# Performance work log

Hardware: AMD Instinct MI355X
Metric: run time of the kernel (lower is better)

The kernel has to match this reference:

```python
import jax, jax.numpy as jnp
import numpy as np


def conv2d(x, w, b, stride=1, pad=0):
    out = jax.lax.conv_general_dilated(
        x, w, (stride, stride), ((pad, pad), (pad, pad)),
        dimension_numbers=('NCHW', 'OIHW', 'NCHW'))
    return out + b[None, :, None, None]


def maxpool2(x):
    return jax.lax.reduce_window(x, -jnp.inf, jax.lax.max,
                                 (1, 1, 2, 2), (1, 1, 2, 2), 'VALID')


def pixel_match_(x, y):
    # x, y: (1, C, H, W). 9-way shifted squared-diff cost volume.
    _, C, H, W = x.shape
    yc = y[0, :, 1:H - 1, 1:W - 1]
    inner = []
    for dh in range(3):
        for dw in range(3):
            tmp = x[0, :, dh:dh + H - 2, dw:dw + W - 2] - yc
            inner.append(jnp.sum(tmp * tmp, axis=0))
    inner = jnp.stack(inner)  # (9, H-2, W-2)
    diff = jnp.zeros((9, H, W), x.dtype).at[:, 1:H - 1, 1:W - 1].set(inner)
    diff = 1.0 / jnp.sqrt(diff + 0.01)
    diff = diff / jnp.sum(diff, axis=0, keepdims=True)
    return diff[None]  # (1, 9, H, W)


def positional(H, W, dtype):
    h = jnp.arange(H, dtype=dtype)
    w = jnp.arange(W, dtype=dtype)
    h = 2.0 * h / h[-1] - 1.0
    w = 2.0 * w / w[-1] - 1.0
    ph = jnp.broadcast_to(h[:, None], (H, W))
    pw = jnp.broadcast_to(w[None, :], (H, W))
    return jnp.stack([ph, pw])[None]  # (1, 2, H, W)


def pixel_match(x, y):
    return jnp.concatenate(
        [pixel_match_(x, y), pixel_match_(y, x),
         positional(x.shape[2], x.shape[3], x.dtype)], axis=1)


def adaptive_max_pool3(x):
    # torch adaptive_max_pool2d semantics: bin i spans [floor(i*H/3), ceil((i+1)*H/3))
    _, C, H, W = x.shape
    rows = []
    for i in range(3):
        hs, he = (i * H) // 3, -((-(i + 1) * H) // 3)
        cols = []
        for j in range(3):
            ws, we = (j * W) // 3, -((-(j + 1) * W) // 3)
            cols.append(jnp.max(x[:, :, hs:he, ws:we], axis=(2, 3)))
        rows.append(jnp.stack(cols, axis=-1))
    return jnp.stack(rows, axis=-2)  # (1, C, 3, 3)


def setup_inputs() -> dict:
    key = jax.random.key(0)
    ks = jax.random.split(key, 16)
    f = jnp.float32
    H = W = 1024
    s = 0.05
    return {
        'x1': jax.random.normal(ks[0], (3, H, W), f),
        'x2': jax.random.normal(ks[1], (3, H, W), f),
        'enc_w': jax.random.normal(ks[2], (24, 3, 3, 3), f) * s,
        'enc_b': jax.random.normal(ks[3], (24,), f) * s,
        'embed_w': jax.random.normal(ks[4], (32, 24, 1, 1), f) * s,
        'embed_b': jax.random.normal(ks[5], (32,), f) * s,
        'dense_w': jax.random.normal(ks[6], (8, 32, 5, 5), f) * s,
        'dense_b': jax.random.normal(ks[7], (8,), f) * s,
        'f1_w': jax.random.normal(ks[8], (64, 48, 1, 1), f) * s,
        'f1_b': jax.random.normal(ks[9], (64,), f) * s,
        'f2_w': jax.random.normal(ks[10], (128, 64, 3, 3), f) * s,
        'f2_b': jax.random.normal(ks[11], (128,), f) * s,
        'f3_w': jax.random.normal(ks[12], (6, 128), f) * s,
        'f3_b': jax.random.normal(ks[13], (6,), f) * s,
    }


def reference(x1, x2, enc_w, enc_b, embed_w, embed_b, dense_w, dense_b,
              f1_w, f1_b, f2_w, f2_b, f3_w, f3_b):
    def coding(x):
        x = x[None]  # (1,3,H,W)
        x = jax.lax.stop_gradient(conv2d(x, enc_w, enc_b, pad=1))  # frozen encoder
        x = conv2d(x, embed_w, embed_b)
        return maxpool2(x)

    c1 = coding(x1)
    c2 = coding(x2)
    level1 = maxpool2(pixel_match(c1, c2))
    p1 = maxpool2(c1)
    p2 = maxpool2(c2)
    level2 = pixel_match(p1, p2)
    dense = jax.nn.leaky_relu(conv2d(p1 - p2, dense_w, dense_b, pad=2))
    x = jnp.concatenate([level1, level2, dense], axis=1)  # (1,48,H/4,W/4)
    x = conv2d(x, f1_w, f1_b)
    x = adaptive_max_pool3(x)
    x = conv2d(x, f2_w, f2_b).reshape(1, 128)
    tmp = jnp.sum(x * x) + 0.001
    x = x / jnp.sqrt(tmp)
    x = (x @ f3_w.T + f3_b).reshape(2, 3)
    x = jnp.concatenate([x, jnp.zeros((1, 3), x.dtype)], axis=0)
    return jnp.eye(3, dtype=x.dtype) + jnp.clip(x, -0.11, 0.11) + x * 0.01
```

## Files before the change

### kernel.cpp

```cpp
#include <hip/hip_runtime.h>
#include <math.h>


__global__ void fuse_weights_kernel(const float* __restrict__ enc_w,
                                    const float* __restrict__ enc_b,
                                    const float* __restrict__ embed_w,
                                    const float* __restrict__ embed_b,
                                    float* __restrict__ weff_t,
                                    float* __restrict__ beff) {
    int t = threadIdx.x;
    for (int idx = t; idx < 27 * 32; idx += blockDim.x) {
        int r = idx >> 5, o = idx & 31;
        float s = 0.f;
        for (int k = 0; k < 24; ++k) s += embed_w[o * 24 + k] * enc_w[k * 27 + r];
        weff_t[idx] = s;
    }
    if (t < 32) {
        float s = embed_b[t];
        for (int k = 0; k < 24; ++k) s += embed_w[t * 24 + k] * enc_b[k];
        beff[t] = s;
    }
}

__global__ __launch_bounds__(256) void coding_kernel(
    const float* __restrict__ x1, const float* __restrict__ x2,
    const float* __restrict__ weff_t, const float* __restrict__ beff,
    float* __restrict__ c1, float* __restrict__ c2,
    float* __restrict__ p1, float* __restrict__ p2) {
    int tx = threadIdx.x, ty = threadIdx.y;
    int img = blockIdx.z;
    const float* x = img ? x2 : x1;
    float* c = img ? c2 : c1;
    float* p = img ? p2 : p1;
    int Y = blockIdx.y * 16 + ty;
    int cx = blockIdx.x * 16 + tx;
    int X0 = 2 * cx;
    bool interior = (blockIdx.y > 0 && blockIdx.y < 63 &&
                     blockIdx.x > 0 && blockIdx.x < 31);
    float acc0[32], acc1[32];
#pragma unroll
    for (int o = 0; o < 32; ++o) {
        acc0[o] = beff[o];
        acc1[o] = acc0[o];
    }
#pragma unroll 1
    for (int ci = 0; ci < 3; ++ci) {
        float in[3][4];
        const float* xc = x + ci * 1048576;
        if (interior) {
#pragma unroll
            for (int r = 0; r < 3; ++r) {
                const float* row = xc + (Y - 1 + r) * 1024 + X0 - 1;
#pragma unroll
                for (int q = 0; q < 4; ++q) in[r][q] = row[q];
            }
        } else {
#pragma unroll
            for (int r = 0; r < 3; ++r)
#pragma unroll
                for (int q = 0; q < 4; ++q) {
                    int gy = Y - 1 + r, gx = X0 - 1 + q;
                    in[r][q] = (gy >= 0 && gy < 1024 && gx >= 0 && gx < 1024)
                                   ? xc[gy * 1024 + gx]
                                   : 0.f;
                }
        }
#pragma unroll
        for (int ky = 0; ky < 3; ++ky)
#pragma unroll
            for (int kx = 0; kx < 3; ++kx) {
                const float* wrow = weff_t + (ci * 9 + ky * 3 + kx) * 32;
                float xa = in[ky][kx];
                float xb = in[ky][kx + 1];
#pragma unroll
                for (int o = 0; o < 32; ++o) {
                    float wv = wrow[o];
                    acc0[o] = fmaf(wv, xa, acc0[o]);
                    acc1[o] = fmaf(wv, xb, acc1[o]);
                }
            }
    }
#pragma unroll
    for (int o = 0; o < 32; ++o) {
        float m = fmaxf(acc0[o], acc1[o]);
        acc0[o] = fmaxf(m, __shfl_xor(m, 16, 64));
    }
    int cpix = (Y >> 1) * 512 + cx;
    if ((ty & 1) == 0) {
        float4* cd = (float4*)(c + cpix * 32);
#pragma unroll
        for (int q = 0; q < 8; ++q)
            cd[q] = make_float4(acc0[4 * q], acc0[4 * q + 1], acc0[4 * q + 2],
                                acc0[4 * q + 3]);
    }
#pragma unroll
    for (int o = 0; o < 32; ++o) {
        float v = fmaxf(acc0[o], __shfl_xor(acc0[o], 1, 64));
        acc0[o] = fmaxf(v, __shfl_xor(v, 32, 64));
    }
    if (((ty & 3) == 0) && ((tx & 1) == 0)) {
        int ppix = (Y >> 2) * 256 + (cx >> 1);
        float4* pd = (float4*)(p + ppix * 32);
#pragma unroll
        for (int q = 0; q < 8; ++q)
            pd[q] = make_float4(acc0[4 * q], acc0[4 * q + 1], acc0[4 * q + 2],
                                acc0[4 * q + 3]);
    }
}

__global__ __launch_bounds__(256) void pm512_pool_kernel(
    const float* __restrict__ c1, const float* __restrict__ c2,
    float* __restrict__ feat) {
    int tid = threadIdx.x;
    int quad = tid & 3;
    int pl = tid >> 2;
    int px = pl & 7, py = pl >> 3;
    int sw = blockIdx.x * 8 + px;
    int sh = blockIdx.y * 8 + py;
    bool interior = (sh >= 1 && sh <= 510 && sw >= 1 && sw <= 510);
    const float* b1 = c1 + (sh * 512 + sw) * 32 + quad * 8;
    const float* b2 = c2 + (sh * 512 + sw) * 32 + quad * 8;
    float a1[9], a2[9];
#pragma unroll
    for (int k = 0; k < 9; ++k) { a1[k] = 0.f; a2[k] = 0.f; }
    if (interior) {
        float4 y1a = ((const float4*)b1)[0], y1b = ((const float4*)b1)[1];
        float4 y2a = ((const float4*)b2)[0], y2b = ((const float4*)b2)[1];
#pragma unroll
        for (int dh = -1; dh <= 1; ++dh)
#pragma unroll
            for (int dw = -1; dw <= 1; ++dw) {
                int k = (dh + 1) * 3 + (dw + 1);
                const float4* n1 = (const float4*)(b1 + (dh * 512 + dw) * 32);
                const float4* n2 = (const float4*)(b2 + (dh * 512 + dw) * 32);
                float4 na = n1[0], nA = n1[1], nb = n2[0], nB = n2[1];
                float s1 = a1[k], s2 = a2[k], t;
                t = na.x - y2a.x; s1 = fmaf(t, t, s1);
                t = na.y - y2a.y; s1 = fmaf(t, t, s1);
                t = na.z - y2a.z; s1 = fmaf(t, t, s1);
                t = na.w - y2a.w; s1 = fmaf(t, t, s1);
                t = nA.x - y2b.x; s1 = fmaf(t, t, s1);
                t = nA.y - y2b.y; s1 = fmaf(t, t, s1);
                t = nA.z - y2b.z; s1 = fmaf(t, t, s1);
                t = nA.w - y2b.w; s1 = fmaf(t, t, s1);
                t = nb.x - y1a.x; s2 = fmaf(t, t, s2);
                t = nb.y - y1a.y; s2 = fmaf(t, t, s2);
                t = nb.z - y1a.z; s2 = fmaf(t, t, s2);
                t = nb.w - y1a.w; s2 = fmaf(t, t, s2);
                t = nB.x - y1b.x; s2 = fmaf(t, t, s2);
                t = nB.y - y1b.y; s2 = fmaf(t, t, s2);
                t = nB.z - y1b.z; s2 = fmaf(t, t, s2);
                t = nB.w - y1b.w; s2 = fmaf(t, t, s2);
                a1[k] = s1;
                a2[k] = s2;
            }
    }
#pragma unroll
    for (int k = 0; k < 9; ++k) {
        a1[k] += __shfl_xor(a1[k], 1, 64);
        a1[k] += __shfl_xor(a1[k], 2, 64);
        a2[k] += __shfl_xor(a2[k], 1, 64);
        a2[k] += __shfl_xor(a2[k], 2, 64);
    }
    float d[20];
    if (interior) {
        float s1 = 0.f, s2 = 0.f;
#pragma unroll
        for (int k = 0; k < 9; ++k) {
            a1[k] = 1.0f / sqrtf(a1[k] + 0.01f);
            a2[k] = 1.0f / sqrtf(a2[k] + 0.01f);
            s1 += a1[k];
            s2 += a2[k];
        }
        float i1 = 1.0f / s1, i2 = 1.0f / s2;
#pragma unroll
        for (int k = 0; k < 9; ++k) {
            d[k] = a1[k] * i1;
            d[9 + k] = a2[k] * i2;
        }
    } else {
#pragma unroll
        for (int k = 0; k < 18; ++k) d[k] = 1.0f / 9.0f;
    }
#pragma unroll
    for (int k = 0; k < 18; ++k) {
        float v = fmaxf(d[k], __shfl_xor(d[k], 4, 64));
        d[k] = fmaxf(v, __shfl_xor(v, 32, 64));
    }
    d[18] = 2.0f * (sh | 1) / 511.0f - 1.0f;
    d[19] = 2.0f * (sw | 1) / 511.0f - 1.0f;
    if ((tid & 36) == 0) {
        int opix = (sh >> 1) * 256 + (sw >> 1);
#pragma unroll
        for (int j = 0; j < 5; ++j)
            feat[(quad * 5 + j) * 65536 + opix] = d[quad * 5 + j];
    }
}

__global__ __launch_bounds__(256) void pm256_kernel(
    const float* __restrict__ p1, const float* __restrict__ p2,
    float* __restrict__ feat) {
    int tid = threadIdx.x;
    int quad = tid & 3;
    int pl = tid >> 2;
    int px = pl & 7, py = pl >> 3;
    int w = blockIdx.x * 8 + px;
    int h = blockIdx.y * 8 + py;
    bool interior = (h >= 1 && h <= 254 && w >= 1 && w <= 254);
    const float* b1 = p1 + (h * 256 + w) * 32 + quad * 8;
    const float* b2 = p2 + (h * 256 + w) * 32 + quad * 8;
    float a1[9], a2[9];
#pragma unroll
    for (int k = 0; k < 9; ++k) { a1[k] = 0.f; a2[k] = 0.f; }
    if (interior) {
        float4 y1a = ((const float4*)b1)[0], y1b = ((const float4*)b1)[1];
        float4 y2a = ((const float4*)b2)[0], y2b = ((const float4*)b2)[1];
#pragma unroll
        for (int dh = -1; dh <= 1; ++dh)
#pragma unroll
            for (int dw = -1; dw <= 1; ++dw) {
                int k = (dh + 1) * 3 + (dw + 1);
                const float4* n1 = (const float4*)(b1 + (dh * 256 + dw) * 32);
                const float4* n2 = (const float4*)(b2 + (dh * 256 + dw) * 32);
                float4 na = n1[0], nA = n1[1], nb = n2[0], nB = n2[1];
                float s1 = a1[k], s2 = a2[k], t;
                t = na.x - y2a.x; s1 = fmaf(t, t, s1);
                t = na.y - y2a.y; s1 = fmaf(t, t, s1);
                t = na.z - y2a.z; s1 = fmaf(t, t, s1);
                t = na.w - y2a.w; s1 = fmaf(t, t, s1);
                t = nA.x - y2b.x; s1 = fmaf(t, t, s1);
                t = nA.y - y2b.y; s1 = fmaf(t, t, s1);
                t = nA.z - y2b.z; s1 = fmaf(t, t, s1);
                t = nA.w - y2b.w; s1 = fmaf(t, t, s1);
                t = nb.x - y1a.x; s2 = fmaf(t, t, s2);
                t = nb.y - y1a.y; s2 = fmaf(t, t, s2);
                t = nb.z - y1a.z; s2 = fmaf(t, t, s2);
                t = nb.w - y1a.w; s2 = fmaf(t, t, s2);
                t = nB.x - y1b.x; s2 = fmaf(t, t, s2);
                t = nB.y - y1b.y; s2 = fmaf(t, t, s2);
                t = nB.z - y1b.z; s2 = fmaf(t, t, s2);
                t = nB.w - y1b.w; s2 = fmaf(t, t, s2);
                a1[k] = s1;
                a2[k] = s2;
            }
    }
#pragma unroll
    for (int k = 0; k < 9; ++k) {
        a1[k] += __shfl_xor(a1[k], 1, 64);
        a1[k] += __shfl_xor(a1[k], 2, 64);
        a2[k] += __shfl_xor(a2[k], 1, 64);
        a2[k] += __shfl_xor(a2[k], 2, 64);
    }
    float d[20];
    if (interior) {
        float s1 = 0.f, s2 = 0.f;
#pragma unroll
        for (int k = 0; k < 9; ++k) {
            a1[k] = 1.0f / sqrtf(a1[k] + 0.01f);
            a2[k] = 1.0f / sqrtf(a2[k] + 0.01f);
            s1 += a1[k];
            s2 += a2[k];
        }
        float i1 = 1.0f / s1, i2 = 1.0f / s2;
#pragma unroll
        for (int k = 0; k < 9; ++k) {
            d[k] = a1[k] * i1;
            d[9 + k] = a2[k] * i2;
        }
    } else {
#pragma unroll
        for (int k = 0; k < 18; ++k) d[k] = 1.0f / 9.0f;
    }
    d[18] = 2.0f * h / 255.0f - 1.0f;
    d[19] = 2.0f * w / 255.0f - 1.0f;
    int pix = h * 256 + w;
#pragma unroll
    for (int j = 0; j < 5; ++j)
        feat[(20 + quad * 5 + j) * 65536 + pix] = d[quad * 5 + j];
}

__global__ __launch_bounds__(256) void dense_part_kernel(
    const float* __restrict__ p1, const float* __restrict__ p2,
    const float* __restrict__ dw, float* __restrict__ part) {
    __shared__ float sdiff[4 * 1296];
    __shared__ float sw[4 * 8 * 28];
    int tx = threadIdx.x, ty = threadIdx.y;
    int tid = ty * 16 + tx;
    int bz = blockIdx.z;
    int h0 = blockIdx.y * 32, w0 = blockIdx.x * 32;
    for (int idx = tid; idx < 1296; idx += 256) {
        int yy = idx / 36, xx = idx % 36;
        int gy = h0 + yy - 2, gx = w0 + xx - 2;
        float4 dv = make_float4(0.f, 0.f, 0.f, 0.f);
        if (gy >= 0 && gy < 256 && gx >= 0 && gx < 256) {
            const float4* q1 =
                (const float4*)(p1 + (gy * 256 + gx) * 32 + bz * 4);
            const float4* q2 =
                (const float4*)(p2 + (gy * 256 + gx) * 32 + bz * 4);
            float4 v1 = q1[0], v2 = q2[0];
            dv = make_float4(v1.x - v2.x, v1.y - v2.y, v1.z - v2.z, v1.w - v2.w);
        }
        sdiff[0 * 1296 + idx] = dv.x;
        sdiff[1 * 1296 + idx] = dv.y;
        sdiff[2 * 1296 + idx] = dv.z;
        sdiff[3 * 1296 + idx] = dv.w;
    }
    for (int idx = tid; idx < 4 * 8 * 28; idx += 256) {
        int ci = idx / 224, r = idx % 224;
        int o = r / 28, k = r % 28;
        sw[idx] = (k < 25) ? dw[o * 800 + (bz * 4 + ci) * 25 + k] : 0.f;
    }
    __syncthreads();
    float acc[4][8];
#pragma unroll
    for (int pq = 0; pq < 4; ++pq)
#pragma unroll
        for (int o = 0; o < 8; ++o) acc[pq][o] = 0.f;
    for (int ci = 0; ci < 4; ++ci) {
        float patch[6][6];
#pragma unroll
        for (int yy = 0; yy < 6; ++yy) {
            const float* rowp = &sdiff[ci * 1296 + (2 * ty + yy) * 36 + 2 * tx];
#pragma unroll
            for (int cpair = 0; cpair < 3; ++cpair) {
                float2 lp = *(const float2*)&rowp[2 * cpair];
                patch[yy][2 * cpair] = lp.x;
                patch[yy][2 * cpair + 1] = lp.y;
            }
        }
#pragma unroll
        for (int o = 0; o < 8; ++o) {
            float wreg[28];
            const float4* wp = (const float4*)&sw[(ci * 8 + o) * 28];
#pragma unroll
            for (int q = 0; q < 7; ++q) {
                float4 wv = wp[q];
                wreg[4 * q] = wv.x;
                wreg[4 * q + 1] = wv.y;
                wreg[4 * q + 2] = wv.z;
                wreg[4 * q + 3] = wv.w;
            }
#pragma unroll
            for (int ky = 0; ky < 5; ++ky)
#pragma unroll
                for (int kx = 0; kx < 5; ++kx) {
                    float wv = wreg[ky * 5 + kx];
#pragma unroll
                    for (int pq = 0; pq < 4; ++pq)
                        acc[pq][o] = fmaf(
                            wv, patch[ky + (pq >> 1)][kx + (pq & 1)], acc[pq][o]);
                }
        }
    }
#pragma unroll
    for (int pq = 0; pq < 4; ++pq) {
        int h = h0 + 2 * ty + (pq >> 1), w = w0 + 2 * tx + (pq & 1);
        int pix = h * 256 + w;
#pragma unroll
        for (int o = 0; o < 8; ++o)
            part[bz * 524288 + o * 65536 + pix] = acc[pq][o];
    }
}

__global__ __launch_bounds__(256) void dense_reduce_kernel(
    const float* __restrict__ part, const float* __restrict__ db,
    float* __restrict__ feat) {
    int idx = blockIdx.x * 256 + threadIdx.x;
    int o = idx >> 16;
    float s = db[o];
#pragma unroll
    for (int z = 0; z < 8; ++z) s += part[z * 524288 + idx];
    float v = (s >= 0.f) ? s : 0.01f * s;
    feat[40 * 65536 + idx] = v;
}

__global__ __launch_bounds__(256) void f1_kernel(
    const float* __restrict__ feat, const float* __restrict__ f1w,
    const float* __restrict__ f1b, float* __restrict__ out) {
    __shared__ float sw[1536];
    __shared__ float sb[32];
    int og = blockIdx.y;
    int tid = threadIdx.x;
    for (int i = tid; i < 1536; i += 256) sw[i] = f1w[og * 1536 + i];
    if (tid < 32) sb[tid] = f1b[og * 32 + tid];
    __syncthreads();
    int pix = blockIdx.x * 256 + tid;
    float f[48];
#pragma unroll
    for (int c = 0; c < 48; ++c) f[c] = feat[c * 65536 + pix];
#pragma unroll
    for (int o = 0; o < 32; ++o) {
        float a = sb[o];
        const float4* wv = (const float4*)&sw[o * 48];
#pragma unroll
        for (int c4 = 0; c4 < 12; ++c4) {
            float4 ww = wv[c4];
            a = fmaf(ww.x, f[c4 * 4], a);
            a = fmaf(ww.y, f[c4 * 4 + 1], a);
            a = fmaf(ww.z, f[c4 * 4 + 2], a);
            a = fmaf(ww.w, f[c4 * 4 + 3], a);
        }
        out[(og * 32 + o) * 65536 + pix] = a;
    }
}

__global__ __launch_bounds__(256) void pool3_kernel(
    const float* __restrict__ f1out, float* __restrict__ pooled) {
    int b = blockIdx.x;
    int c = b / 9, ij = b % 9, i = ij / 3, j = ij % 3;
    int hs = (i * 256) / 3, he = ((i + 1) * 256 + 2) / 3;
    int ws = (j * 256) / 3, we = ((j + 1) * 256 + 2) / 3;
    const float* src = f1out + c * 65536;
    int nh = he - hs, nw = we - ws, tot = nh * nw;
    float m = -INFINITY;
    for (int t = threadIdx.x; t < tot; t += 256) {
        int r = t / nw, q = t - r * nw;
        m = fmaxf(m, src[(hs + r) * 256 + (ws + q)]);
    }
    for (int off = 32; off > 0; off >>= 1) m = fmaxf(m, __shfl_down(m, off, 64));
    __shared__ float red[4];
    if ((threadIdx.x & 63) == 0) red[threadIdx.x >> 6] = m;
    __syncthreads();
    if (threadIdx.x == 0)
        pooled[b] = fmaxf(fmaxf(red[0], red[1]), fmaxf(red[2], red[3]));
}

__global__ __launch_bounds__(128) void final_kernel(
    const float* __restrict__ pooled, const float* __restrict__ f2w,
    const float* __restrict__ f2b, const float* __restrict__ f3w,
    const float* __restrict__ f3b, float* __restrict__ out) {
    __shared__ float xn[128];
    __shared__ float red[2];
    __shared__ float ov[6];
    int t = threadIdx.x;
    float a = f2b[t];
    for (int c = 0; c < 64; ++c)
#pragma unroll
        for (int k = 0; k < 9; ++k)
            a = fmaf(f2w[t * 576 + c * 9 + k], pooled[c * 9 + k], a);
    float sq = a * a;
    for (int off = 32; off > 0; off >>= 1) sq += __shfl_down(sq, off, 64);
    if ((t & 63) == 0) red[t >> 6] = sq;
    __syncthreads();
    float tmp = red[0] + red[1] + 0.001f;
    float scale = 1.0f / sqrtf(tmp);
    xn[t] = a * scale;
    __syncthreads();
    if (t < 6) {
        float o = f3b[t];
        for (int k = 0; k < 128; ++k) o = fmaf(f3w[t * 128 + k], xn[k], o);
        ov[t] = o;
    }
    __syncthreads();
    if (t < 9) {
        int r = t / 3, cc = t % 3;
        float v = 0.f;
        if (r < 2) {
            float x = ov[r * 3 + cc];
            float cl = fminf(fmaxf(x, -0.11f), 0.11f);
            v = cl + 0.01f * x;
        }
        if (r == cc) v += 1.0f;
        out[t] = v;
    }
}

extern "C" void kernel_launch(void* const* d_in, const int* in_sizes, int n_in,
                              void* d_out, int out_size, void* d_ws,
                              size_t ws_size, hipStream_t stream) {
    const float* x1 = (const float*)d_in[0];
    const float* x2 = (const float*)d_in[1];
    const float* enc_w = (const float*)d_in[2];
    const float* enc_b = (const float*)d_in[3];
    const float* embed_w = (const float*)d_in[4];
    const float* embed_b = (const float*)d_in[5];
    const float* dense_w = (const float*)d_in[6];
    const float* dense_b = (const float*)d_in[7];
    const float* f1_w = (const float*)d_in[8];
    const float* f1_b = (const float*)d_in[9];
    const float* f2_w = (const float*)d_in[10];
    const float* f2_b = (const float*)d_in[11];
    const float* f3_w = (const float*)d_in[12];
    const float* f3_b = (const float*)d_in[13];

    float* ws = (float*)d_ws;
    float* weff_t = ws;
    float* beff = ws + 864;
    float* c1 = ws + 1024;
    float* c2 = c1 + 8388608;
    float* p1 = c2 + 8388608;
    float* p2 = p1 + 2097152;
    float* feat = p2 + 2097152;
    float* pooled = feat + 3145728;
    float* f1o = c1;
    float* part = c2;

    fuse_weights_kernel<<<1, 256, 0, stream>>>(enc_w, enc_b, embed_w, embed_b,
                                               weff_t, beff);
    coding_kernel<<<dim3(32, 64, 2), dim3(16, 16), 0, stream>>>(
        x1, x2, weff_t, beff, c1, c2, p1, p2);
    pm512_pool_kernel<<<dim3(64, 64), 256, 0, stream>>>(c1, c2, feat);
    pm256_kernel<<<dim3(32, 32), 256, 0, stream>>>(p1, p2, feat);
    dense_part_kernel<<<dim3(8, 8, 8), dim3(16, 16), 0, stream>>>(
        p1, p2, dense_w, part);
    dense_reduce_kernel<<<2048, 256, 0, stream>>>(part, dense_b, feat);
    f1_kernel<<<dim3(256, 2), 256, 0, stream>>>(feat, f1_w, f1_b, f1o);
    pool3_kernel<<<576, 256, 0, stream>>>(f1o, pooled);
    final_kernel<<<1, 128, 0, stream>>>(pooled, f2_w, f2_b, f3_w, f3_b,
                                        (float*)d_out);
}
```

Measured before the change: 184.9 us.

## Merge pixel-match and dense conv into one launch; fold dense reduce into f1

Combines the 512-level pixel-match, the 256-level pixel-match and the dense partial-conv kernels into a single kernel that dispatches on block index, so three launches become one and their blocks can run together. The dense reduction with bias and leaky-relu moves into f1_kernel, which now sums the 8 partial buffers itself instead of reading a precomputed feature plane. The partial buffer moves to its own workspace region because it can no longer alias c2, which the fused kernel still reads. The cost is that every block reserves the dense path's shared memory, which may lower occupancy for the pixel-match blocks, and f1 does extra reads (each output-group block re-reads the partials).

```diff
diff --git a/kernel.cpp b/kernel.cpp
--- a/kernel.cpp
+++ b/kernel.cpp
@@ -108,274 +108,272 @@
     }
 }
 
-__global__ __launch_bounds__(256) void pm512_pool_kernel(
+__global__ __launch_bounds__(256) void mid_kernel(
     const float* __restrict__ c1, const float* __restrict__ c2,
-    float* __restrict__ feat) {
+    const float* __restrict__ p1, const float* __restrict__ p2,
+    const float* __restrict__ dw, float* __restrict__ feat,
+    float* __restrict__ part) {
+    __shared__ float smem[4 * 1296 + 4 * 8 * 28];
+    int bid = blockIdx.x;
     int tid = threadIdx.x;
-    int quad = tid & 3;
-    int pl = tid >> 2;
-    int px = pl & 7, py = pl >> 3;
-    int sw = blockIdx.x * 8 + px;
-    int sh = blockIdx.y * 8 + py;
-    bool interior = (sh >= 1 && sh <= 510 && sw >= 1 && sw <= 510);
-    const float* b1 = c1 + (sh * 512 + sw) * 32 + quad * 8;
-    const float* b2 = c2 + (sh * 512 + sw) * 32 + quad * 8;
-    float a1[9], a2[9];
-#pragma unroll
-    for (int k = 0; k < 9; ++k) { a1[k] = 0.f; a2[k] = 0.f; }
-    if (interior) {
-        float4 y1a = ((const float4*)b1)[0], y1b = ((const float4*)b1)[1];
-        float4 y2a = ((const float4*)b2)[0], y2b = ((const float4*)b2)[1];
-#pragma unroll
-        for (int dh = -1; dh <= 1; ++dh)
-#pragma unroll
-            for (int dw = -1; dw <= 1; ++dw) {
-                int k = (dh + 1) * 3 + (dw + 1);
-                const float4* n1 = (const float4*)(b1 + (dh * 512 + dw) * 32);
-                const float4* n2 = (const float4*)(b2 + (dh * 512 + dw) * 32);
-                float4 na = n1[0], nA = n1[1], nb = n2[0], nB = n2[1];
-                float s1 = a1[k], s2 = a2[k], t;
-                t = na.x - y2a.x; s1 = fmaf(t, t, s1);
-                t = na.y - y2a.y; s1 = fmaf(t, t, s1);
-                t = na.z - y2a.z; s1 = fmaf(t, t, s1);
-                t = na.w - y2a.w; s1 = fmaf(t, t, s1);
-                t = nA.x - y2b.x; s1 = fmaf(t, t, s1);
-                t = nA.y - y2b.y; s1 = fmaf(t, t, s1);
-                t = nA.z - y2b.z; s1 = fmaf(t, t, s1);
-                t = nA.w - y2b.w; s1 = fmaf(t, t, s1);
-                t = nb.x - y1a.x; s2 = fmaf(t, t, s2);
-                t = nb.y - y1a.y; s2 = fmaf(t, t, s2);
-                t = nb.z - y1a.z; s2 = fmaf(t, t, s2);
-                t = nb.w - y1a.w; s2 = fmaf(t, t, s2);
-                t = nB.x - y1b.x; s2 = fmaf(t, t, s2);
-                t = nB.y - y1b.y; s2 = fmaf(t, t, s2);
-                t = nB.z - y1b.z; s2 = fmaf(t, t, s2);
-                t = nB.w - y1b.w; s2 = fmaf(t, t, s2);
-                a1[k] = s1;
-                a2[k] = s2;
-            }
-    }
-#pragma unroll
-    for (int k = 0; k < 9; ++k) {
-        a1[k] += __shfl_xor(a1[k], 1, 64);
-        a1[k] += __shfl_xor(a1[k], 2, 64);
-        a2[k] += __shfl_xor(a2[k], 1, 64);
-        a2[k] += __shfl_xor(a2[k], 2, 64);
-    }
-    float d[20];
-    if (interior) {
-        float s1 = 0.f, s2 = 0.f;
+    if (bid < 4096) {
+        int bx = bid & 63, by = bid >> 6;
+        int quad = tid & 3;
+        int pl = tid >> 2;
+        int px = pl & 7, py = pl >> 3;
+        int sw = bx * 8 + px;
+        int sh = by * 8 + py;
+        bool interior = (sh >= 1 && sh <= 510 && sw >= 1 && sw <= 510);
+        const float* b1 = c1 + (sh * 512 + sw) * 32 + quad * 8;
+        const float* b2 = c2 + (sh * 512 + sw) * 32 + quad * 8;
+        float a1[9], a2[9];
+#pragma unroll
+        for (int k = 0; k < 9; ++k) { a1[k] = 0.f; a2[k] = 0.f; }
+        if (interior) {
+            float4 y1a = ((const float4*)b1)[0], y1b = ((const float4*)b1)[1];
+            float4 y2a = ((const float4*)b2)[0], y2b = ((const float4*)b2)[1];
+#pragma unroll
+            for (int dh = -1; dh <= 1; ++dh)
+#pragma unroll
+                for (int dwp = -1; dwp <= 1; ++dwp) {
+                    int k = (dh + 1) * 3 + (dwp + 1);
+                    const float4* n1 =
+                        (const float4*)(b1 + (dh * 512 + dwp) * 32);
+                    const float4* n2 =
+                        (const float4*)(b2 + (dh * 512 + dwp) * 32);
+                    float4 na = n1[0], nA = n1[1], nb = n2[0], nB = n2[1];
+                    float s1 = a1[k], s2 = a2[k], t;
+                    t = na.x - y2a.x; s1 = fmaf(t, t, s1);
+                    t = na.y - y2a.y; s1 = fmaf(t, t, s1);
+                    t = na.z - y2a.z; s1 = fmaf(t, t, s1);
+                    t = na.w - y2a.w; s1 = fmaf(t, t, s1);
+                    t = nA.x - y2b.x; s1 = fmaf(t, t, s1);
+                    t = nA.y - y2b.y; s1 = fmaf(t, t, s1);
+                    t = nA.z - y2b.z; s1 = fmaf(t, t, s1);
+                    t = nA.w - y2b.w; s1 = fmaf(t, t, s1);
+                    t = nb.x - y1a.x; s2 = fmaf(t, t, s2);
+                    t = nb.y - y1a.y; s2 = fmaf(t, t, s2);
+                    t = nb.z - y1a.z; s2 = fmaf(t, t, s2);
+                    t = nb.w - y1a.w; s2 = fmaf(t, t, s2);
+                    t = nB.x - y1b.x; s2 = fmaf(t, t, s2);
+                    t = nB.y - y1b.y; s2 = fmaf(t, t, s2);
+                    t = nB.z - y1b.z; s2 = fmaf(t, t, s2);
+                    t = nB.w - y1b.w; s2 = fmaf(t, t, s2);
+                    a1[k] = s1;
+                    a2[k] = s2;
+                }
+        }
 #pragma unroll
         for (int k = 0; k < 9; ++k) {
-            a1[k] = 1.0f / sqrtf(a1[k] + 0.01f);
-            a2[k] = 1.0f / sqrtf(a2[k] + 0.01f);
-            s1 += a1[k];
-            s2 += a2[k];
-        }
-        float i1 = 1.0f / s1, i2 = 1.0f / s2;
+            a1[k] += __shfl_xor(a1[k], 1, 64);
+            a1[k] += __shfl_xor(a1[k], 2, 64);
+            a2[k] += __shfl_xor(a2[k], 1, 64);
+            a2[k] += __shfl_xor(a2[k], 2, 64);
+        }
+        float d[20];
+        if (interior) {
+            float s1 = 0.f, s2 = 0.f;
+#pragma unroll
+            for (int k = 0; k < 9; ++k) {
+                a1[k] = 1.0f / sqrtf(a1[k] + 0.01f);
+                a2[k] = 1.0f / sqrtf(a2[k] + 0.01f);
+                s1 += a1[k];
+                s2 += a2[k];
+            }
+            float i1 = 1.0f / s1, i2 = 1.0f / s2;
+#pragma unroll
+            for (int k = 0; k < 9; ++k) {
+                d[k] = a1[k] * i1;
+                d[9 + k] = a2[k] * i2;
+            }
+        } else {
+#pragma unroll
+            for (int k = 0; k < 18; ++k) d[k] = 1.0f / 9.0f;
+        }
+#pragma unroll
+        for (int k = 0; k < 18; ++k) {
+            float v = fmaxf(d[k], __shfl_xor(d[k], 4, 64));
+            d[k] = fmaxf(v, __shfl_xor(v, 32, 64));
+        }
+        d[18] = 2.0f * (sh | 1) / 511.0f - 1.0f;
+        d[19] = 2.0f * (sw | 1) / 511.0f - 1.0f;
+        if ((tid & 36) == 0) {
+            int opix = (sh >> 1) * 256 + (sw >> 1);
+#pragma unroll
+            for (int j = 0; j < 5; ++j)
+                feat[(quad * 5 + j) * 65536 + opix] = d[quad * 5 + j];
+        }
+    } else if (bid < 5120) {
+        int i = bid - 4096;
+        int bx = i & 31, by = i >> 5;
+        int quad = tid & 3;
+        int pl = tid >> 2;
+        int px = pl & 7, py = pl >> 3;
+        int w = bx * 8 + px;
+        int h = by * 8 + py;
+        bool interior = (h >= 1 && h <= 254 && w >= 1 && w <= 254);
+        const float* b1 = p1 + (h * 256 + w) * 32 + quad * 8;
+        const float* b2 = p2 + (h * 256 + w) * 32 + quad * 8;
+        float a1[9], a2[9];
+#pragma unroll
+        for (int k = 0; k < 9; ++k) { a1[k] = 0.f; a2[k] = 0.f; }
+        if (interior) {
+            float4 y1a = ((const float4*)b1)[0], y1b = ((const float4*)b1)[1];
+            float4 y2a = ((const float4*)b2)[0], y2b = ((const float4*)b2)[1];
+#pragma unroll
+            for (int dh = -1; dh <= 1; ++dh)
+#pragma unroll
+                for (int dwp = -1; dwp <= 1; ++dwp) {
+                    int k = (dh + 1) * 3 + (dwp + 1);
+                    const float4* n1 =
+                        (const float4*)(b1 + (dh * 256 + dwp) * 32);
+                    const float4* n2 =
+                        (const float4*)(b2 + (dh * 256 + dwp) * 32);
+                    float4 na = n1[0], nA = n1[1], nb = n2[0], nB = n2[1];
+                    float s1 = a1[k], s2 = a2[k], t;
+                    t = na.x - y2a.x; s1 = fmaf(t, t, s1);
+                    t = na.y - y2a.y; s1 = fmaf(t, t, s1);
+                    t = na.z - y2a.z; s1 = fmaf(t, t, s1);
+                    t = na.w - y2a.w; s1 = fmaf(t, t, s1);
+                    t = nA.x - y2b.x; s1 = fmaf(t, t, s1);
+                    t = nA.y - y2b.y; s1 = fmaf(t, t, s1);
+                    t = nA.z - y2b.z; s1 = fmaf(t, t, s1);
+                    t = nA.w - y2b.w; s1 = fmaf(t, t, s1);
+                    t = nb.x - y1a.x; s2 = fmaf(t, t, s2);
+                    t = nb.y - y1a.y; s2 = fmaf(t, t, s2);
+                    t = nb.z - y1a.z; s2 = fmaf(t, t, s2);
+                    t = nb.w - y1a.w; s2 = fmaf(t, t, s2);
+                    t = nB.x - y1b.x; s2 = fmaf(t, t, s2);
+                    t = nB.y - y1b.y; s2 = fmaf(t, t, s2);
+                    t = nB.z - y1b.z; s2 = fmaf(t, t, s2);
+                    t = nB.w - y1b.w; s2 = fmaf(t, t, s2);
+                    a1[k] = s1;
+                    a2[k] = s2;
+                }
+        }
 #pragma unroll
         for (int k = 0; k < 9; ++k) {
-            d[k] = a1[k] * i1;
-            d[9 + k] = a2[k] * i2;
-        }
+            a1[k] += __shfl_xor(a1[k], 1, 64);
+            a1[k] += __shfl_xor(a1[k], 2, 64);
+            a2[k] += __shfl_xor(a2[k], 1, 64);
+            a2[k] += __shfl_xor(a2[k], 2, 64);
+        }
+        float d[20];
+        if (interior) {
+            float s1 = 0.f, s2 = 0.f;
+#pragma unroll
+            for (int k = 0; k < 9; ++k) {
+                a1[k] = 1.0f / sqrtf(a1[k] + 0.01f);
+                a2[k] = 1.0f / sqrtf(a2[k] + 0.01f);
+                s1 += a1[k];
+                s2 += a2[k];
+            }
+            float i1 = 1.0f / s1, i2 = 1.0f / s2;
+#pragma unroll
+            for (int k = 0; k < 9; ++k) {
+                d[k] = a1[k] * i1;
+                d[9 + k] = a2[k] * i2;
+            }
+        } else {
+#pragma unroll
+            for (int k = 0; k < 18; ++k) d[k] = 1.0f / 9.0f;
+        }
+        d[18] = 2.0f * h / 255.0f - 1.0f;
+        d[19] = 2.0f * w / 255.0f - 1.0f;
+        int pix = h * 256 + w;
+#pragma unroll
+        for (int j = 0; j < 5; ++j)
+            feat[(20 + quad * 5 + j) * 65536 + pix] = d[quad * 5 + j];
     } else {
-#pragma unroll
-        for (int k = 0; k < 18; ++k) d[k] = 1.0f / 9.0f;
-    }
-#pragma unroll
-    for (int k = 0; k < 18; ++k) {
-        float v = fmaxf(d[k], __shfl_xor(d[k], 4, 64));
-        d[k] = fmaxf(v, __shfl_xor(v, 32, 64));
-    }
-    d[18] = 2.0f * (sh | 1) / 511.0f - 1.0f;
-    d[19] = 2.0f * (sw | 1) / 511.0f - 1.0f;
-    if ((tid & 36) == 0) {
-        int opix = (sh >> 1) * 256 + (sw >> 1);
-#pragma unroll
-        for (int j = 0; j < 5; ++j)
-            feat[(quad * 5 + j) * 65536 + opix] = d[quad * 5 + j];
-    }
-}
-
-__global__ __launch_bounds__(256) void pm256_kernel(
-    const float* __restrict__ p1, const float* __restrict__ p2,
-    float* __restrict__ feat) {
-    int tid = threadIdx.x;
-    int quad = tid & 3;
-    int pl = tid >> 2;
-    int px = pl & 7, py = pl >> 3;
-    int w = blockIdx.x * 8 + px;
-    int h = blockIdx.y * 8 + py;
-    bool interior = (h >= 1 && h <= 254 && w >= 1 && w <= 254);
-    const float* b1 = p1 + (h * 256 + w) * 32 + quad * 8;
-    const float* b2 = p2 + (h * 256 + w) * 32 + quad * 8;
-    float a1[9], a2[9];
-#pragma unroll
-    for (int k = 0; k < 9; ++k) { a1[k] = 0.f; a2[k] = 0.f; }
-    if (interior) {
-        float4 y1a = ((const float4*)b1)[0], y1b = ((const float4*)b1)[1];
-        float4 y2a = ((const float4*)b2)[0], y2b = ((const float4*)b2)[1];
-#pragma unroll
-        for (int dh = -1; dh <= 1; ++dh)
-#pragma unroll
-            for (int dw = -1; dw <= 1; ++dw) {
-                int k = (dh + 1) * 3 + (dw + 1);
-                const float4* n1 = (const float4*)(b1 + (dh * 256 + dw) * 32);
-                const float4* n2 = (const float4*)(b2 + (dh * 256 + dw) * 32);
-                float4 na = n1[0], nA = n1[1], nb = n2[0], nB = n2[1];
-                float s1 = a1[k], s2 = a2[k], t;
-                t = na.x - y2a.x; s1 = fmaf(t, t, s1);
-                t = na.y - y2a.y; s1 = fmaf(t, t, s1);
-                t = na.z - y2a.z; s1 = fmaf(t, t, s1);
-                t = na.w - y2a.w; s1 = fmaf(t, t, s1);
-                t = nA.x - y2b.x; s1 = fmaf(t, t, s1);
-                t = nA.y - y2b.y; s1 = fmaf(t, t, s1);
-                t = nA.z - y2b.z; s1 = fmaf(t, t, s1);
-                t = nA.w - y2b.w; s1 = fmaf(t, t, s1);
-                t = nb.x - y1a.x; s2 = fmaf(t, t, s2);
-                t = nb.y - y1a.y; s2 = fmaf(t, t, s2);
-                t = nb.z - y1a.z; s2 = fmaf(t, t, s2);
-                t = nb.w - y1a.w; s2 = fmaf(t, t, s2);
-                t = nB.x - y1b.x; s2 = fmaf(t, t, s2);
-                t = nB.y - y1b.y; s2 = fmaf(t, t, s2);
-                t = nB.z - y1b.z; s2 = fmaf(t, t, s2);
-                t = nB.w - y1b.w; s2 = fmaf(t, t, s2);
-                a1[k] = s1;
-                a2[k] = s2;
-            }
-    }
-#pragma unroll
-    for (int k = 0; k < 9; ++k) {
-        a1[k] += __shfl_xor(a1[k], 1, 64);
-        a1[k] += __shfl_xor(a1[k], 2, 64);
-        a2[k] += __shfl_xor(a2[k], 1, 64);
-        a2[k] += __shfl_xor(a2[k], 2, 64);
-    }
-    float d[20];
-    if (interior) {
-        float s1 = 0.f, s2 = 0.f;
-#pragma unroll
-        for (int k = 0; k < 9; ++k) {
-            a1[k] = 1.0f / sqrtf(a1[k] + 0.01f);
-            a2[k] = 1.0f / sqrtf(a2[k] + 0.01f);
-            s1 += a1[k];
-            s2 += a2[k];
-        }
-        float i1 = 1.0f / s1, i2 = 1.0f / s2;
-#pragma unroll
-        for (int k = 0; k < 9; ++k) {
-            d[k] = a1[k] * i1;
-            d[9 + k] = a2[k] * i2;
-        }
-    } else {
-#pragma unroll
-        for (int k = 0; k < 18; ++k) d[k] = 1.0f / 9.0f;
-    }
-    d[18] = 2.0f * h / 255.0f - 1.0f;
-    d[19] = 2.0f * w / 255.0f - 1.0f;
-    int pix = h * 256 + w;
-#pragma unroll
-    for (int j = 0; j < 5; ++j)
-        feat[(20 + quad * 5 + j) * 65536 + pix] = d[quad * 5 + j];
-}
-
-__global__ __launch_bounds__(256) void dense_part_kernel(
-    const float* __restrict__ p1, const float* __restrict__ p2,
-    const float* __restrict__ dw, float* __restrict__ part) {
-    __shared__ float sdiff[4 * 1296];
-    __shared__ float sw[4 * 8 * 28];
-    int tx = threadIdx.x, ty = threadIdx.y;
-    int tid = ty * 16 + tx;
-    int bz = blockIdx.z;
-    int h0 = blockIdx.y * 32, w0 = blockIdx.x * 32;
-    for (int idx = tid; idx < 1296; idx += 256) {
-        int yy = idx / 36, xx = idx % 36;
-        int gy = h0 + yy - 2, gx = w0 + xx - 2;
-        float4 dv = make_float4(0.f, 0.f, 0.f, 0.f);
-        if (gy >= 0 && gy < 256 && gx >= 0 && gx < 256) {
-            const float4* q1 =
-                (const float4*)(p1 + (gy * 256 + gx) * 32 + bz * 4);
-            const float4* q2 =
-                (const float4*)(p2 + (gy * 256 + gx) * 32 + bz * 4);
-            float4 v1 = q1[0], v2 = q2[0];
-            dv = make_float4(v1.x - v2.x, v1.y - v2.y, v1.z - v2.z, v1.w - v2.w);
-        }
-        sdiff[0 * 1296 + idx] = dv.x;
-        sdiff[1 * 1296 + idx] = dv.y;
-        sdiff[2 * 1296 + idx] = dv.z;
-        sdiff[3 * 1296 + idx] = dv.w;
-    }
-    for (int idx = tid; idx < 4 * 8 * 28; idx += 256) {
-        int ci = idx / 224, r = idx % 224;
-        int o = r / 28, k = r % 28;
-        sw[idx] = (k < 25) ? dw[o * 800 + (bz * 4 + ci) * 25 + k] : 0.f;
-    }
-    __syncthreads();
-    float acc[4][8];
-#pragma unroll
-    for (int pq = 0; pq < 4; ++pq)
-#pragma unroll
-        for (int o = 0; o < 8; ++o) acc[pq][o] = 0.f;
-    for (int ci = 0; ci < 4; ++ci) {
-        float patch[6][6];
-#pragma unroll
-        for (int yy = 0; yy < 6; ++yy) {
-            const float* rowp = &sdiff[ci * 1296 + (2 * ty + yy) * 36 + 2 * tx];
-#pragma unroll
-            for (int cpair = 0; cpair < 3; ++cpair) {
-                float2 lp = *(const float2*)&rowp[2 * cpair];
-                patch[yy][2 * cpair] = lp.x;
-                patch[yy][2 * cpair + 1] = lp.y;
-            }
-        }
-#pragma unroll
-        for (int o = 0; o < 8; ++o) {
-            float wreg[28];
-            const float4* wp = (const float4*)&sw[(ci * 8 + o) * 28];
-#pragma unroll
-            for (int q = 0; q < 7; ++q) {
-                float4 wv = wp[q];
-                wreg[4 * q] = wv.x;
-                wreg[4 * q + 1] = wv.y;
-                wreg[4 * q + 2] = wv.z;
-                wreg[4 * q + 3] = wv.w;
-            }
-#pragma unroll
-            for (int ky = 0; ky < 5; ++ky)
-#pragma unroll
-                for (int kx = 0; kx < 5; ++kx) {
-                    float wv = wreg[ky * 5 + kx];
-#pragma unroll
-                    for (int pq = 0; pq < 4; ++pq)
-                        acc[pq][o] = fmaf(
-                            wv, patch[ky + (pq >> 1)][kx + (pq & 1)], acc[pq][o]);
+        float* sdiff = smem;
+        float* sw = smem + 4 * 1296;
+        int i = bid - 5120;
+        int bz = i >> 6;
+        int rem = i & 63;
+        int by = rem >> 3, bx = rem & 7;
+        int tx = tid & 15, ty = tid >> 4;
+        int h0 = by * 32, w0 = bx * 32;
+        for (int idx = tid; idx < 1296; idx += 256) {
+            int yy = idx / 36, xx = idx % 36;
+            int gy = h0 + yy - 2, gx = w0 + xx - 2;
+            float4 dv = make_float4(0.f, 0.f, 0.f, 0.f);
+            if (gy >= 0 && gy < 256 && gx >= 0 && gx < 256) {
+                const float4* q1 =
+                    (const float4*)(p1 + (gy * 256 + gx) * 32 + bz * 4);
+                const float4* q2 =
+                    (const float4*)(p2 + (gy * 256 + gx) * 32 + bz * 4);
+                float4 v1 = q1[0], v2 = q2[0];
+                dv = make_float4(v1.x - v2.x, v1.y - v2.y, v1.z - v2.z,
+                                 v1.w - v2.w);
+            }
+            sdiff[0 * 1296 + idx] = dv.x;
+            sdiff[1 * 1296 + idx] = dv.y;
+            sdiff[2 * 1296 + idx] = dv.z;
+            sdiff[3 * 1296 + idx] = dv.w;
+        }
+        for (int idx = tid; idx < 4 * 8 * 28; idx += 256) {
+            int ci = idx / 224, r = idx % 224;
+            int o = r / 28, k = r % 28;
+            sw[idx] = (k < 25) ? dw[o * 800 + (bz * 4 + ci) * 25 + k] : 0.f;
+        }
+        __syncthreads();
+        float acc[4][8];
+#pragma unroll
+        for (int pq = 0; pq < 4; ++pq)
+#pragma unroll
+            for (int o = 0; o < 8; ++o) acc[pq][o] = 0.f;
+        for (int ci = 0; ci < 4; ++ci) {
+            float patch[6][6];
+#pragma unroll
+            for (int yy = 0; yy < 6; ++yy) {
+                const float* rowp =
+                    &sdiff[ci * 1296 + (2 * ty + yy) * 36 + 2 * tx];
+#pragma unroll
+                for (int cpair = 0; cpair < 3; ++cpair) {
+                    float2 lp = *(const float2*)&rowp[2 * cpair];
+                    patch[yy][2 * cpair] = lp.x;
+                    patch[yy][2 * cpair + 1] = lp.y;
                 }
-        }
-    }
-#pragma unroll
-    for (int pq = 0; pq < 4; ++pq) {
-        int h = h0 + 2 * ty + (pq >> 1), w = w0 + 2 * tx + (pq & 1);
-        int pix = h * 256 + w;
-#pragma unroll
-        for (int o = 0; o < 8; ++o)
-            part[bz * 524288 + o * 65536 + pix] = acc[pq][o];
-    }
-}
-
-__global__ __launch_bounds__(256) void dense_reduce_kernel(
-    const float* __restrict__ part, const float* __restrict__ db,
-    float* __restrict__ feat) {
-    int idx = blockIdx.x * 256 + threadIdx.x;
-    int o = idx >> 16;
-    float s = db[o];
-#pragma unroll
-    for (int z = 0; z < 8; ++z) s += part[z * 524288 + idx];
-    float v = (s >= 0.f) ? s : 0.01f * s;
-    feat[40 * 65536 + idx] = v;
+            }
+#pragma unroll
+            for (int o = 0; o < 8; ++o) {
+                float wreg[28];
+                const float4* wp = (const float4*)&sw[(ci * 8 + o) * 28];
+#pragma unroll
+                for (int q = 0; q < 7; ++q) {
+                    float4 wv = wp[q];
+                    wreg[4 * q] = wv.x;
+                    wreg[4 * q + 1] = wv.y;
+                    wreg[4 * q + 2] = wv.z;
+                    wreg[4 * q + 3] = wv.w;
+                }
+#pragma unroll
+                for (int ky = 0; ky < 5; ++ky)
+#pragma unroll
+                    for (int kx = 0; kx < 5; ++kx) {
+                        float wv = wreg[ky * 5 + kx];
+#pragma unroll
+                        for (int pq = 0; pq < 4; ++pq)
+                            acc[pq][o] =
+                                fmaf(wv, patch[ky + (pq >> 1)][kx + (pq & 1)],
+                                     acc[pq][o]);
+                    }
+            }
+        }
+#pragma unroll
+        for (int pq = 0; pq < 4; ++pq) {
+            int h = h0 + 2 * ty + (pq >> 1), w = w0 + 2 * tx + (pq & 1);
+            int pix = h * 256 + w;
+#pragma unroll
+            for (int o = 0; o < 8; ++o)
+                part[bz * 524288 + o * 65536 + pix] = acc[pq][o];
+        }
+    }
 }
 
 __global__ __launch_bounds__(256) void f1_kernel(
-    const float* __restrict__ feat, const float* __restrict__ f1w,
+    const float* __restrict__ feat, const float* __restrict__ part,
+    const float* __restrict__ db, const float* __restrict__ f1w,
     const float* __restrict__ f1b, float* __restrict__ out) {
     __shared__ float sw[1536];
     __shared__ float sb[32];
@@ -387,7 +385,14 @@
     int pix = blockIdx.x * 256 + tid;
     float f[48];
 #pragma unroll
-    for (int c = 0; c < 48; ++c) f[c] = feat[c * 65536 + pix];
+    for (int c = 0; c < 40; ++c) f[c] = feat[c * 65536 + pix];
+#pragma unroll
+    for (int o = 0; o < 8; ++o) {
+        float s = db[o];
+#pragma unroll
+        for (int z = 0; z < 8; ++z) s += part[z * 524288 + o * 65536 + pix];
+        f[40 + o] = (s >= 0.f) ? s : 0.01f * s;
+    }
 #pragma unroll
     for (int o = 0; o < 32; ++o) {
         float a = sb[o];
@@ -492,19 +497,16 @@
     float* p2 = p1 + 2097152;
     float* feat = p2 + 2097152;
     float* pooled = feat + 3145728;
+    float* part = pooled + 1024;
     float* f1o = c1;
-    float* part = c2;
 
     fuse_weights_kernel<<<1, 256, 0, stream>>>(enc_w, enc_b, embed_w, embed_b,
                                                weff_t, beff);
     coding_kernel<<<dim3(32, 64, 2), dim3(16, 16), 0, stream>>>(
         x1, x2, weff_t, beff, c1, c2, p1, p2);
-    pm512_pool_kernel<<<dim3(64, 64), 256, 0, stream>>>(c1, c2, feat);
-    pm256_kernel<<<dim3(32, 32), 256, 0, stream>>>(p1, p2, feat);
-    dense_part_kernel<<<dim3(8, 8, 8), dim3(16, 16), 0, stream>>>(
-        p1, p2, dense_w, part);
-    dense_reduce_kernel<<<2048, 256, 0, stream>>>(part, dense_b, feat);
-    f1_kernel<<<dim3(256, 2), 256, 0, stream>>>(feat, f1_w, f1_b, f1o);
+    mid_kernel<<<5632, 256, 0, stream>>>(c1, c2, p1, p2, dense_w, feat, part);
+    f1_kernel<<<dim3(256, 2), 256, 0, stream>>>(feat, part, dense_b, f1_w,
+                                                f1_b, f1o);
     pool3_kernel<<<576, 256, 0, stream>>>(f1o, pooled);
     final_kernel<<<1, 128, 0, stream>>>(pooled, f2_w, f2_b, f3_w, f3_b,
                                         (float*)d_out);
```

After: 175.1 us (median of 2 runs). 1.06x faster.
